# Optimization experiments

Hardware: AMD Instinct MI355X
Metric: run time of the kernel (lower is better)

The kernel has to match this reference:

```python
import jax, jax.numpy as jnp
from jax import lax
import numpy as np

B = 32768
H = 7
W = 7
EMB = 64
NUM_ACTIONS = 7
HIDDEN = 128
CNN_OUT = 64 * 3 * 3  # 576, from 7x7 input through the conv/pool stack


def setup_inputs() -> dict:
    key = jax.random.key(0)
    ks = jax.random.split(key, 20)
    frame = jax.random.randint(ks[0], (2, B, H, W, 3), 0, 11, dtype=jnp.int32)
    carried_col = jax.random.randint(ks[1], (2, B, 1), 0, 6, dtype=jnp.int32)
    carried_obj = jax.random.randint(ks[2], (2, B, 1), 0, 11, dtype=jnp.int32)

    def w(k, shape):
        return (jax.random.normal(k, shape, jnp.float32) * 0.05)

    return {
        "frame": frame,
        "carried_col": carried_col,
        "carried_obj": carried_obj,
        "conv1_w": w(ks[3], (16, 3, 2, 2)),  "conv1_b": jnp.zeros((16,), jnp.float32),
        "conv2_w": w(ks[4], (32, 16, 2, 2)), "conv2_b": jnp.zeros((32,), jnp.float32),
        "conv3_w": w(ks[5], (64, 32, 2, 2)), "conv3_b": jnp.zeros((64,), jnp.float32),
        "proj_w": w(ks[6], (EMB, CNN_OUT + 2)), "proj_b": jnp.zeros((EMB,), jnp.float32),
        "h1_w": w(ks[7], (HIDDEN, EMB * 2 + 4)), "h1_b": jnp.zeros((HIDDEN,), jnp.float32),
        "ln_g": jnp.ones((HIDDEN,), jnp.float32), "ln_b": jnp.zeros((HIDDEN,), jnp.float32),
        "h2_w": w(ks[8], (HIDDEN, HIDDEN)), "h2_b": jnp.zeros((HIDDEN,), jnp.float32),
        "h3_w": w(ks[9], (NUM_ACTIONS, HIDDEN)), "h3_b": jnp.zeros((NUM_ACTIONS,), jnp.float32),
    }


def _conv(x, wgt, b):
    # Conv2d(kernel=2, padding=1), NCHW
    y = lax.conv_general_dilated(x, wgt, (1, 1), [(1, 1), (1, 1)],
                                 dimension_numbers=("NCHW", "OIHW", "NCHW"))
    return y + b[None, :, None, None]


def _maxpool2(x):
    # MaxPool2d(2): window 2, stride 2, floor (VALID)
    return lax.reduce_window(x, -jnp.inf, lax.max, (1, 1, 2, 2), (1, 1, 2, 2), "VALID")


def _encode(fr, cc, co, p):
    x = fr.transpose(0, 3, 1, 2).astype(jnp.float32)  # [B,3,H,W]
    x = _maxpool2(jax.nn.relu(_conv(x, p["conv1_w"], p["conv1_b"])))  # [B,16,4,4]
    x = _maxpool2(jax.nn.relu(_conv(x, p["conv2_w"], p["conv2_b"])))  # [B,32,2,2]
    x = jax.nn.relu(_conv(x, p["conv3_w"], p["conv3_b"]))             # [B,64,3,3]
    feats = x.reshape(x.shape[0], -1)                                  # [B,576]
    carried = jnp.concatenate([cc, co], axis=-1).astype(jnp.float32)   # [B,2]
    comb = jnp.concatenate([feats, carried], axis=1)                   # [B,578]
    return jax.nn.relu(comb @ p["proj_w"].T + p["proj_b"])            # [B,64]


def _dir_pos(fr):
    # vectorized first-match of frame[...,0]==10 in row-major order
    b = fr.shape[0]
    mask = (fr[..., 0] == 10).reshape(b, -1)             # [B, H*W]
    has = jnp.any(mask, axis=-1)                         # [B]
    idx = jnp.argmax(mask, axis=-1)                      # first True (row-major)
    y = idx // W
    x = idx % W
    ch2 = fr[..., 2].reshape(b, -1)
    d_raw = jnp.take_along_axis(ch2, idx[:, None], axis=1)[:, 0] % 4
    d = jnp.where(has, d_raw, 0)                         # [B] int
    pos = jnp.stack([y.astype(jnp.float32) / (H - 1),
                     x.astype(jnp.float32) / (W - 1)], axis=-1)
    pos = jnp.where(has[:, None], pos, jnp.float32(0.5))  # [B,2]
    return d, pos


def _forward(frame, carried_col, carried_obj, p):
    curr_f, next_f = frame[0], frame[1]
    curr_emb = _encode(curr_f, carried_col[0], carried_obj[0], p)
    next_emb = _encode(next_f, carried_col[1], carried_obj[1], p)
    cd, cpos = _dir_pos(curr_f)
    nd, npos = _dir_pos(next_f)
    delta = ((nd - cd + 4) % 4).astype(jnp.float32)
    angle = delta * (2.0 * 3.14159 / 4.0)  # matches source constant
    dir_delta = jnp.stack([jnp.sin(angle), jnp.cos(angle)], axis=-1)  # [B,2]
    pos_delta = npos - cpos                                           # [B,2]
    comb = jnp.concatenate([curr_emb, next_emb, dir_delta, pos_delta], axis=-1)  # [B,132]
    h = comb @ p["h1_w"].T + p["h1_b"]
    mu = h.mean(-1, keepdims=True)
    var = ((h - mu) ** 2).mean(-1, keepdims=True)
    h = (h - mu) * lax.rsqrt(var + 1e-5) * p["ln_g"] + p["ln_b"]
    h = jax.nn.relu(h)  # dropout = identity in eval
    h = jax.nn.relu(h @ p["h2_w"].T + p["h2_b"])
    return h @ p["h3_w"].T + p["h3_b"]  # [B, num_actions]


def reference(frame, carried_col, carried_obj,
              conv1_w, conv1_b, conv2_w, conv2_b, conv3_w, conv3_b,
              proj_w, proj_b, h1_w, h1_b, ln_g, ln_b,
              h2_w, h2_b, h3_w, h3_b):
    p = dict(conv1_w=conv1_w, conv1_b=conv1_b, conv2_w=conv2_w, conv2_b=conv2_b,
             conv3_w=conv3_w, conv3_b=conv3_b, proj_w=proj_w, proj_b=proj_b,
             h1_w=h1_w, h1_b=h1_b, ln_g=ln_g, ln_b=ln_b,
             h2_w=h2_w, h2_b=h2_b, h3_w=h3_w, h3_b=h3_b)
    return _forward(frame, carried_col, carried_obj, p)
```

## Files before the change

### kernel.cpp

```cpp
#include <hip/hip_runtime.h>
#include <hip/hip_bf16.h>

#define BATCH 32768

typedef unsigned short u16;
typedef unsigned int u32;
typedef __attribute__((ext_vector_type(8))) short bf16x8;
typedef __attribute__((ext_vector_type(4))) float f32x4;

__device__ __forceinline__ float bf2f(u16 u) {
    union { u32 u; float f; } c; c.u = ((u32)u) << 16; return c.f;
}
__device__ __forceinline__ u16 f2bf(float f) {
    union { float f; u32 u; } c; c.f = f;
    u32 x = c.u;
    u32 r = (x + 0x7fffu + ((x >> 16) & 1u)) >> 16;
    return (u16)r;
}
__device__ __forceinline__ u16 i2bf(int v) {
    union { float f; u32 u; } c; c.f = (float)v;
    return (u16)(c.u >> 16);
}

__global__ __launch_bounds__(256) void k0_prep(const float* __restrict__ pw,
        const float* __restrict__ w2, const float* __restrict__ w3,
        const float* __restrict__ h2w, const float* __restrict__ h1w,
        const float* __restrict__ w1,
        u16* __restrict__ pwT, u16* __restrict__ w2r, u16* __restrict__ w3r,
        u16* __restrict__ h2hi, u16* __restrict__ h2lo,
        u16* __restrict__ h1hi, u16* __restrict__ h1lo,
        u16* __restrict__ w1hi, u16* __restrict__ w1lo) {
    int idx = blockIdx.x * 256 + threadIdx.x;
    if (idx < 38912) {
        int j = idx / 608, kk = idx - j * 608;
        float v = 0.f;
        if (kk < 576) {
            int p = kk >> 6, oc = kk & 63;
            v = pw[j * 578 + oc * 9 + p];
        } else if (kk < 578) {
            v = pw[j * 578 + kk];
        }
        pwT[idx] = f2bf(v);
    } else if (idx < 40960) {
        int i = idx - 38912;
        int oc = i >> 6, rem = i & 63, tap = rem >> 4, ic = rem & 15;
        w2r[i] = f2bf(w2[oc * 64 + ic * 4 + tap]);
    } else if (idx < 49152) {
        int i = idx - 40960;
        int oc = i >> 7, rem = i & 127, tap = rem >> 5, ic = rem & 31;
        w3r[i] = f2bf(w3[oc * 128 + ic * 4 + tap]);
    } else if (idx < 65536) {
        int i = idx - 49152;
        float v = h2w[i];
        u16 hi = f2bf(v);
        h2hi[i] = hi;
        h2lo[i] = f2bf(v - bf2f(hi));
    } else if (idx < 86016) {
        int i = idx - 65536;
        int j = i / 160, k = i - j * 160;
        float v = (k < 132) ? h1w[j * 132 + k] : 0.f;
        u16 hi = f2bf(v);
        h1hi[i] = hi;
        h1lo[i] = f2bf(v - bf2f(hi));
    } else if (idx < 86528) {
        int i = idx - 86016;
        int oc = i >> 5, k = i & 31;
        int ky = k >> 3, kx = (k >> 2) & 1, c = k & 3;
        float v = (ky < 2 && c < 3) ? w1[oc * 12 + c * 4 + ky * 2 + kx] : 0.f;
        u16 hi = f2bf(v);
        w1hi[i] = hi;
        w1lo[i] = f2bf(v - bf2f(hi));
    }
}

__global__ __launch_bounds__(512, 4) void kall(const int* __restrict__ frame,
        const u16* __restrict__ w1hi, const u16* __restrict__ w1lo,
        const float* __restrict__ b1,
        const u16* __restrict__ w2r, const float* __restrict__ b2,
        const u16* __restrict__ w3r, const float* __restrict__ b3,
        const int* __restrict__ ccol, const int* __restrict__ cobj,
        const u16* __restrict__ pwT, const float* __restrict__ pb,
        const u16* __restrict__ h1hi, const u16* __restrict__ h1lo,
        const float* __restrict__ h1b,
        const float* __restrict__ lng, const float* __restrict__ lnb,
        const u16* __restrict__ h2hi, const u16* __restrict__ h2lo,
        const float* __restrict__ h2b,
        const float* __restrict__ h3w, const float* __restrict__ h3b,
        float* __restrict__ out) {
    __shared__ u16 lds[22784];
    __shared__ float4 fdirL[32];
    u16* p2L    = lds;
    u16* p1L    = lds + 4096;
    u16* frL4   = lds + 12288;
    u16* featL  = lds + 4096;
    u16* combHi = lds;
    u16* combLo = lds + 2688;
    float* hL   = (float*)(lds + 5376);
    u16* hLhi   = lds + 9600;
    u16* hLlo   = lds + 12288;

    int t = threadIdx.x;
    int l = t & 63;
    int wv = t >> 6;
    int col = l & 15;
    int kg = l >> 4;
    int wq = wv & 3, wh = wv >> 2;
    int b0 = blockIdx.x * 16;

    #pragma unroll
    for (int i = 0; i < 3; ++i) {
        int o = i * 512 + t;
        if (o < 1312) *(uint4*)(frL4 + o * 8) = make_uint4(0u, 0u, 0u, 0u);
    }
    __syncthreads();

    #pragma unroll
    for (int i = 0; i < 4; ++i) {
        int c = i * 512 + t;
        if (c < 1568) {
            int le = c / 49, rem = c - le * 49;
            int y = rem / 7, x = rem - y * 7;
            const int* fp = frame
                + ((size_t)b0 + (size_t)(le & 15) + (size_t)(le >> 4) * BATCH) * 147
                + rem * 3;
            int v0 = fp[0], v1 = fp[1], v2 = fp[2];
            uint2 st;
            st.x = (u32)i2bf(v0) | ((u32)i2bf(v1) << 16);
            st.y = (u32)i2bf(v2);
            *(uint2*)(frL4 + le * 328 + (y + 1) * 36 + (x + 1) * 4) = st;
        }
    }
    __syncthreads();

    {
        bf16x8 c1hi = *(const bf16x8*)(w1hi + col * 32 + kg * 8);
        bf16x8 c1lo = *(const bf16x8*)(w1lo + col * 32 + kg * 8);
        float c1b = b1[col];
        bool wr1 = (kg < 2);
        #pragma unroll
        for (int q = 0; q < 4; ++q) {
            int le = wh * 16 + wq * 4 + q;
            const u16* eb = frL4 + le * 328;
            u16* op = p1L + le * 256;
            #pragma unroll
            for (int mt = 0; mt < 4; ++mt) {
                int posA = mt * 16 + col;
                int oy = posA >> 3, ox = posA & 7;
                bf16x8 a;
                if (kg < 2) {
                    const u16* ap = eb + (oy + kg) * 36 + ox * 4;
                    union { uint2 d[2]; bf16x8 v; } uu;
                    uu.d[0] = *(const uint2*)ap;
                    uu.d[1] = *(const uint2*)(ap + 4);
                    a = uu.v;
                } else {
                    #pragma unroll
                    for (int j = 0; j < 8; ++j) a[j] = 0;
                }
                f32x4 acc = {0.f, 0.f, 0.f, 0.f};
                acc = __builtin_amdgcn_mfma_f32_16x16x32_bf16(a, c1hi, acc, 0, 0, 0);
                acc = __builtin_amdgcn_mfma_f32_16x16x32_bf16(a, c1lo, acc, 0, 0, 0);
                float x0 = fmaxf(acc[0] + c1b, 0.f);
                float x1 = fmaxf(acc[1] + c1b, 0.f);
                float x2 = fmaxf(acc[2] + c1b, 0.f);
                float x3 = fmaxf(acc[3] + c1b, 0.f);
                float y0 = fmaxf(x0, x1);
                float y1 = fmaxf(x2, x3);
                float m0 = fmaxf(y0, __shfl_xor(y0, 32, 64));
                float m1 = fmaxf(y1, __shfl_xor(y1, 32, 64));
                if (wr1) {
                    op[(mt * 4 + kg * 2 + 0) * 16 + col] = f2bf(m0);
                    op[(mt * 4 + kg * 2 + 1) * 16 + col] = f2bf(m1);
                }
            }
        }
        {
            int e = wh * 16 + wq * 4 + kg;
            const u16* eb = frL4 + e * 328;
            int best = 49;
            #pragma unroll
            for (int q2 = 0; q2 < 4; ++q2) {
                int cell = col + q2 * 16;
                if (cell < 49) {
                    int y = cell / 7, x = cell - y * 7;
                    u16 v = eb[(y + 1) * 36 + (x + 1) * 4];
                    if (v == (u16)0x4120 && cell < best) best = cell;
                }
            }
            best = min(best, __shfl_xor(best, 1, 64));
            best = min(best, __shfl_xor(best, 2, 64));
            best = min(best, __shfl_xor(best, 4, 64));
            best = min(best, __shfl_xor(best, 8, 64));
            if (col == 0) {
                float dd = 0.f, py = 0.5f, px = 0.5f;
                if (best < 49) {
                    int y = best / 7, x = best - y * 7;
                    u16 c2 = eb[(y + 1) * 36 + (x + 1) * 4 + 2];
                    dd = (float)(((int)bf2f(c2)) & 3);
                    py = (float)y / 6.0f;
                    px = (float)x / 6.0f;
                }
                fdirL[e] = make_float4(dd, py, px, 0.f);
            }
        }
    }
    __syncthreads();

    {
        bf16x8 bfrag[2][2];
        #pragma unroll
        for (int s = 0; s < 2; ++s)
            #pragma unroll
            for (int nt = 0; nt < 2; ++nt)
                bfrag[s][nt] = *(const bf16x8*)(w2r + (nt * 16 + col) * 64 + s * 32 + kg * 8);
        float bias2[2] = { b2[col], b2[16 + col] };
        int oy = col >> 2, ox = col & 3;
        int aoff[2]; bool aok[2];
        #pragma unroll
        for (int s = 0; s < 2; ++s) {
            int tap = 2 * s + (kg >> 1);
            int ky = tap >> 1, kx = tap & 1;
            int iy = oy - 1 + ky, ix = ox - 1 + kx;
            aok[s] = (iy >= 0 && ix >= 0);
            aoff[s] = (iy * 4 + ix) * 16 + (kg & 1) * 8;
        }
        #pragma unroll
        for (int q = 0; q < 4; ++q) {
            int e = wv * 4 + q;
            const u16* pbase = p1L + e * 256;
            bf16x8 a0 = {0,0,0,0,0,0,0,0}, a1 = {0,0,0,0,0,0,0,0};
            if (aok[0]) a0 = *(const bf16x8*)(pbase + aoff[0]);
            if (aok[1]) a1 = *(const bf16x8*)(pbase + aoff[1]);
            f32x4 acc0 = {0.f,0.f,0.f,0.f}, acc1 = {0.f,0.f,0.f,0.f};
            acc0 = __builtin_amdgcn_mfma_f32_16x16x32_bf16(a0, bfrag[0][0], acc0, 0, 0, 0);
            acc1 = __builtin_amdgcn_mfma_f32_16x16x32_bf16(a0, bfrag[0][1], acc1, 0, 0, 0);
            acc0 = __builtin_amdgcn_mfma_f32_16x16x32_bf16(a1, bfrag[1][0], acc0, 0, 0, 0);
            acc1 = __builtin_amdgcn_mfma_f32_16x16x32_bf16(a1, bfrag[1][1], acc1, 0, 0, 0);
            #pragma unroll
            for (int nt = 0; nt < 2; ++nt) {
                f32x4 acc = nt ? acc1 : acc0;
                float b = bias2[nt];
                float m0 = fmaxf(fmaxf(acc[0] + b, 0.f), fmaxf(acc[1] + b, 0.f));
                float m1 = fmaxf(fmaxf(acc[2] + b, 0.f), fmaxf(acc[3] + b, 0.f));
                float p0 = fmaxf(m0, __shfl_xor(m0, 16, 64));
                float p1 = fmaxf(m1, __shfl_xor(m1, 16, 64));
                if ((kg & 1) == 0) {
                    int qq = (kg >> 1) * 2;
                    u16* op = p2L + e * 128 + nt * 16 + col;
                    op[qq * 32]       = f2bf(p0);
                    op[(qq + 1) * 32] = f2bf(p1);
                }
            }
        }
    }
    __syncthreads();

    int colhi = col >> 3, collo = col & 7;
    {
        bf16x8 bfrag[4][4];
        #pragma unroll
        for (int s = 0; s < 4; ++s)
            #pragma unroll
            for (int nt = 0; nt < 4; ++nt)
                bfrag[s][nt] = *(const bf16x8*)(w3r + (nt * 16 + col) * 128 + s * 32 + kg * 8);
        float bias[4];
        #pragma unroll
        for (int nt = 0; nt < 4; ++nt) bias[nt] = b3[nt * 16 + col];

        auto do_tile = [&](int i) {
            int m0 = i * 16;
            int m = m0 + col;
            u32 elem = (u32)(((unsigned long long)(u32)m * 954437177ull) >> 33);
            int p = m - (int)elem * 9;
            int oy = (p * 86) >> 8;
            int ox = p - 3 * oy;
            const u16* pbase = p2L + elem * 128 + kg * 8;
            f32x4 acc[4];
            #pragma unroll
            for (int nt = 0; nt < 4; ++nt) {
                acc[nt][0] = 0.f; acc[nt][1] = 0.f; acc[nt][2] = 0.f; acc[nt][3] = 0.f;
            }
            #pragma unroll
            for (int s = 0; s < 4; ++s) {
                int ky = s >> 1, kx = s & 1;
                int iy = oy - 1 + ky, ix = ox - 1 + kx;
                bf16x8 a = {0,0,0,0,0,0,0,0};
                if (iy >= 0 && iy <= 1 && ix >= 0 && ix <= 1)
                    a = *(const bf16x8*)(pbase + (iy * 2 + ix) * 32);
                #pragma unroll
                for (int nt = 0; nt < 4; ++nt)
                    acc[nt] = __builtin_amdgcn_mfma_f32_16x16x32_bf16(a, bfrag[s][nt], acc[nt], 0, 0, 0);
            }
            #pragma unroll
            for (int r = 0; r < 4; ++r) {
                int mr = m0 + kg * 4 + r;
                u32 er = (u32)(((unsigned long long)(u32)mr * 954437177ull) >> 33);
                int pr = mr - (int)er * 9;
                u16* fb = featL + er * 584 + collo;
                #pragma unroll
                for (int nt = 0; nt < 4; ++nt) {
                    int blk = pr * 8 + nt * 2 + colhi;
                    fb[blk * 8] = f2bf(fmaxf(acc[nt][r] + bias[nt], 0.f));
                }
            }
        };
        do_tile(wv);
        do_tile(8 + wv);
        if (wv < 2) do_tile(16 + wv);
    }
    if (t < 32) {
        int g = b0 + (t >> 4) * BATCH + (t & 15);
        union { u16 s[8]; uint4 q; } b;
        b.s[0] = f2bf((float)ccol[g]);
        b.s[1] = f2bf((float)cobj[g]);
        #pragma unroll
        for (int i = 2; i < 8; ++i) b.s[i] = 0;
        *(uint4*)(featL + t * 584 + 576) = b.q;
    }
    __syncthreads();

    {
        int rh = wv & 1, nf = wv >> 1;
        const u16* arowb = featL + (rh * 16 + col) * 584;
        const u16* brow  = pwT + (nf * 16 + col) * 608 + kg * 8;
        f32x4 accA = {0.f,0.f,0.f,0.f}, accB = {0.f,0.f,0.f,0.f};
        #pragma unroll
        for (int k0 = 0; k0 < 608; k0 += 32) {
            bf16x8 a;
            if (k0 + kg * 8 < 584) {
                a = *(const bf16x8*)(arowb + k0 + kg * 8);
            } else {
                #pragma unroll
                for (int j = 0; j < 8; ++j) a[j] = 0;
            }
            bf16x8 b = *(const bf16x8*)(brow + k0);
            if ((k0 >> 5) & 1)
                accB = __builtin_amdgcn_mfma_f32_16x16x32_bf16(a, b, accB, 0, 0, 0);
            else
                accA = __builtin_amdgcn_mfma_f32_16x16x32_bf16(a, b, accA, 0, 0, 0);
        }
        __syncthreads();
        if (t < 16) {
            float4 f0 = fdirL[t];
            float4 f1 = fdirL[16 + t];
            int delta = (((int)f1.x) - ((int)f0.x) + 4) & 3;
            const float ANG = (float)(2.0 * 3.14159 / 4.0);
            float ang = (float)delta * ANG;
            float xs[4] = { sinf(ang), cosf(ang), f1.y - f0.y, f1.z - f0.z };
            #pragma unroll
            for (int j = 0; j < 4; ++j) {
                u16 hi = f2bf(xs[j]);
                combHi[t * 168 + 128 + j] = hi;
                combLo[t * 168 + 128 + j] = f2bf(xs[j] - bf2f(hi));
            }
        }
        {
            int n = nf * 16 + col;
            float pbv = pb[n];
            #pragma unroll
            for (int r = 0; r < 4; ++r) {
                float v = fmaxf(accA[r] + accB[r] + pbv, 0.f);
                u16 hi = f2bf(v);
                int off = (kg * 4 + r) * 168 + rh * 64 + n;
                combHi[off] = hi;
                combLo[off] = f2bf(v - bf2f(hi));
            }
        }
    }
    __syncthreads();

    {
        const u16* ah = combHi + col * 168 + kg * 8;
        const u16* al = combLo + col * 168 + kg * 8;
        int n = wv * 16 + col;
        const u16* bh = h1hi + n * 160 + kg * 8;
        const u16* bl = h1lo + n * 160 + kg * 8;
        f32x4 accP = {0.f,0.f,0.f,0.f}, accQ = {0.f,0.f,0.f,0.f};
        #pragma unroll
        for (int s = 0; s < 5; ++s) {
            bf16x8 Ah = *(const bf16x8*)(ah + s * 32);
            bf16x8 Al = *(const bf16x8*)(al + s * 32);
            bf16x8 Bh = *(const bf16x8*)(bh + s * 32);
            bf16x8 Bl = *(const bf16x8*)(bl + s * 32);
            accP = __builtin_amdgcn_mfma_f32_16x16x32_bf16(Ah, Bh, accP, 0, 0, 0);
            accQ = __builtin_amdgcn_mfma_f32_16x16x32_bf16(Al, Bh, accQ, 0, 0, 0);
            accQ = __builtin_amdgcn_mfma_f32_16x16x32_bf16(Ah, Bl, accQ, 0, 0, 0);
        }
        float bv = h1b[n];
        #pragma unroll
        for (int r = 0; r < 4; ++r)
            hL[(kg * 4 + r) * 132 + n] = accP[r] + accQ[r] + bv;
    }
    __syncthreads();

    #pragma unroll
    for (int rr = 0; rr < 2; ++rr) {
        int row = wv * 2 + rr;
        float* rp = hL + row * 132 + l * 2;
        float2 v = *(const float2*)rp;
        float s = v.x + v.y;
        s += __shfl_xor(s, 1, 64);
        s += __shfl_xor(s, 2, 64);
        s += __shfl_xor(s, 4, 64);
        s += __shfl_xor(s, 8, 64);
        s += __shfl_xor(s, 16, 64);
        s += __shfl_xor(s, 32, 64);
        float mu = s * (1.0f / 128.0f);
        float d0 = v.x - mu, d1 = v.y - mu;
        float vs = d0 * d0 + d1 * d1;
        vs += __shfl_xor(vs, 1, 64);
        vs += __shfl_xor(vs, 2, 64);
        vs += __shfl_xor(vs, 4, 64);
        vs += __shfl_xor(vs, 8, 64);
        vs += __shfl_xor(vs, 16, 64);
        vs += __shfl_xor(vs, 32, 64);
        float rs = rsqrtf(vs * (1.0f / 128.0f) + 1e-5f);
        float o0 = fmaxf(d0 * rs * lng[l * 2]     + lnb[l * 2],     0.f);
        float o1 = fmaxf(d1 * rs * lng[l * 2 + 1] + lnb[l * 2 + 1], 0.f);
        u16 h0 = f2bf(o0), h1v = f2bf(o1);
        *(u32*)(hLhi + row * 168 + l * 2) = (u32)h0 | ((u32)h1v << 16);
        u16 l0 = f2bf(o0 - bf2f(h0)), l1v = f2bf(o1 - bf2f(h1v));
        *(u32*)(hLlo + row * 168 + l * 2) = (u32)l0 | ((u32)l1v << 16);
    }
    __syncthreads();

    {
        const u16* ah = hLhi + col * 168 + kg * 8;
        const u16* al = hLlo + col * 168 + kg * 8;
        int n = wv * 16 + col;
        const u16* bh = h2hi + n * 128 + kg * 8;
        const u16* bl = h2lo + n * 128 + kg * 8;
        f32x4 accP = {0.f,0.f,0.f,0.f}, accQ = {0.f,0.f,0.f,0.f};
        #pragma unroll
        for (int s = 0; s < 4; ++s) {
            bf16x8 Ah = *(const bf16x8*)(ah + s * 32);
            bf16x8 Al = *(const bf16x8*)(al + s * 32);
            bf16x8 Bh = *(const bf16x8*)(bh + s * 32);
            bf16x8 Bl = *(const bf16x8*)(bl + s * 32);
            accP = __builtin_amdgcn_mfma_f32_16x16x32_bf16(Ah, Bh, accP, 0, 0, 0);
            accQ = __builtin_amdgcn_mfma_f32_16x16x32_bf16(Al, Bh, accQ, 0, 0, 0);
            accQ = __builtin_amdgcn_mfma_f32_16x16x32_bf16(Ah, Bl, accQ, 0, 0, 0);
        }
        float bv = h2b[n];
        #pragma unroll
        for (int r = 0; r < 4; ++r)
            hL[(kg * 4 + r) * 132 + n] = fmaxf(accP[r] + accQ[r] + bv, 0.f);
    }
    __syncthreads();

    if (t < 112) {
        int row = t / 7, j = t - row * 7;
        const float* rp = hL + row * 132;
        const float* wr0 = h3w + j * 128;
        float a0 = h3b[j];
        #pragma unroll 4
        for (int c = 0; c < 32; ++c) {
            float4 v = *(const float4*)(rp + c * 4);
            float4 w = *(const float4*)(wr0 + c * 4);
            a0 += v.x * w.x + v.y * w.y + v.z * w.z + v.w * w.w;
        }
        out[(size_t)(b0 + row) * 7 + j] = a0;
    }
}

extern "C" void kernel_launch(void* const* d_in, const int* in_sizes, int n_in,
                              void* d_out, int out_size, void* d_ws, size_t ws_size,
                              hipStream_t stream) {
    const int*   frame = (const int*)d_in[0];
    const int*   ccol  = (const int*)d_in[1];
    const int*   cobj  = (const int*)d_in[2];
    const float* w1    = (const float*)d_in[3];
    const float* b1    = (const float*)d_in[4];
    const float* w2    = (const float*)d_in[5];
    const float* b2    = (const float*)d_in[6];
    const float* w3    = (const float*)d_in[7];
    const float* b3    = (const float*)d_in[8];
    const float* pw    = (const float*)d_in[9];
    const float* pb    = (const float*)d_in[10];
    const float* h1w   = (const float*)d_in[11];
    const float* h1b   = (const float*)d_in[12];
    const float* lng   = (const float*)d_in[13];
    const float* lnb   = (const float*)d_in[14];
    const float* h2w   = (const float*)d_in[15];
    const float* h2b   = (const float*)d_in[16];
    const float* h3w   = (const float*)d_in[17];
    const float* h3b   = (const float*)d_in[18];
    float* out = (float*)d_out;

    char* ws = (char*)d_ws;
    u16*   pwT      = (u16*)(ws + 0);
    u16*   w2r      = (u16*)(ws + 131072);
    u16*   w3r      = (u16*)(ws + 139264);
    u16*   h2hi     = (u16*)(ws + 163840);
    u16*   h2lo     = (u16*)(ws + 196608);
    u16*   h1hi     = (u16*)(ws + 229376);
    u16*   h1lo     = (u16*)(ws + 270336);
    u16*   w1hi     = (u16*)(ws + 311296);
    u16*   w1lo     = (u16*)(ws + 312320);

    k0_prep<<<340, 256, 0, stream>>>(pw, w2, w3, h2w, h1w, w1,
                                     pwT, w2r, w3r, h2hi, h2lo, h1hi, h1lo,
                                     w1hi, w1lo);
    kall<<<2048, 512, 0, stream>>>(frame, w1hi, w1lo, b1, w2r, b2,
                                   w3r, b3, ccol, cobj, pwT, pb,
                                   h1hi, h1lo, h1b, lng, lnb,
                                   h2hi, h2lo, h2b, h3w, h3b, out);
}
```

Before: 218.3 us.

## Halve block to 8 samples and 256 threads, remapping MLP MFMA tiles

```diff
diff --git a/kernel.cpp b/kernel.cpp
--- a/kernel.cpp
+++ b/kernel.cpp
@@ -73,7 +73,7 @@
     }
 }
 
-__global__ __launch_bounds__(512, 4) void kall(const int* __restrict__ frame,
+__global__ __launch_bounds__(256, 7) void kall(const int* __restrict__ frame,
         const u16* __restrict__ w1hi, const u16* __restrict__ w1lo,
         const float* __restrict__ b1,
         const u16* __restrict__ w2r, const float* __restrict__ b2,
@@ -87,41 +87,40 @@
         const float* __restrict__ h2b,
         const float* __restrict__ h3w, const float* __restrict__ h3b,
         float* __restrict__ out) {
-    __shared__ u16 lds[22784];
-    __shared__ float4 fdirL[32];
+    __shared__ u16 lds[11392];
+    __shared__ float4 fdirL[16];
     u16* p2L    = lds;
-    u16* p1L    = lds + 4096;
-    u16* frL4   = lds + 12288;
-    u16* featL  = lds + 4096;
+    u16* p1L    = lds + 2048;
+    u16* frL4   = lds + 6144;
+    u16* featL  = lds + 2048;
     u16* combHi = lds;
-    u16* combLo = lds + 2688;
-    float* hL   = (float*)(lds + 5376);
-    u16* hLhi   = lds + 9600;
-    u16* hLlo   = lds + 12288;
+    u16* combLo = lds + 1088;
+    float* hL   = (float*)(lds + 2176);
+    u16* hLhi   = lds + 4288;
+    u16* hLlo   = lds + 5376;
 
     int t = threadIdx.x;
     int l = t & 63;
     int wv = t >> 6;
     int col = l & 15;
     int kg = l >> 4;
-    int wq = wv & 3, wh = wv >> 2;
-    int b0 = blockIdx.x * 16;
+    int b0 = blockIdx.x * 8;
 
     #pragma unroll
     for (int i = 0; i < 3; ++i) {
-        int o = i * 512 + t;
-        if (o < 1312) *(uint4*)(frL4 + o * 8) = make_uint4(0u, 0u, 0u, 0u);
+        int o = i * 256 + t;
+        if (o < 656) *(uint4*)(frL4 + o * 8) = make_uint4(0u, 0u, 0u, 0u);
     }
     __syncthreads();
 
     #pragma unroll
     for (int i = 0; i < 4; ++i) {
-        int c = i * 512 + t;
-        if (c < 1568) {
+        int c = i * 256 + t;
+        if (c < 784) {
             int le = c / 49, rem = c - le * 49;
             int y = rem / 7, x = rem - y * 7;
             const int* fp = frame
-                + ((size_t)b0 + (size_t)(le & 15) + (size_t)(le >> 4) * BATCH) * 147
+                + ((size_t)b0 + (size_t)(le & 7) + (size_t)(le >> 3) * BATCH) * 147
                 + rem * 3;
             int v0 = fp[0], v1 = fp[1], v2 = fp[2];
             uint2 st;
@@ -139,7 +138,7 @@
         bool wr1 = (kg < 2);
         #pragma unroll
         for (int q = 0; q < 4; ++q) {
-            int le = wh * 16 + wq * 4 + q;
+            int le = wv * 4 + q;
             const u16* eb = frL4 + le * 328;
             u16* op = p1L + le * 256;
             #pragma unroll
@@ -175,7 +174,7 @@
             }
         }
         {
-            int e = wh * 16 + wq * 4 + kg;
+            int e = wv * 4 + kg;
             const u16* eb = frL4 + e * 328;
             int best = 49;
             #pragma unroll
@@ -305,11 +304,11 @@
             }
         };
         do_tile(wv);
-        do_tile(8 + wv);
-        if (wv < 2) do_tile(16 + wv);
-    }
-    if (t < 32) {
-        int g = b0 + (t >> 4) * BATCH + (t & 15);
+        do_tile(4 + wv);
+        if (wv == 0) do_tile(8);
+    }
+    if (t < 16) {
+        int g = b0 + (t >> 3) * BATCH + (t & 7);
         union { u16 s[8]; uint4 q; } b;
         b.s[0] = f2bf((float)ccol[g]);
         b.s[1] = f2bf((float)cobj[g]);
@@ -320,9 +319,8 @@
     __syncthreads();
 
     {
-        int rh = wv & 1, nf = wv >> 1;
-        const u16* arowb = featL + (rh * 16 + col) * 584;
-        const u16* brow  = pwT + (nf * 16 + col) * 608 + kg * 8;
+        const u16* arowb = featL + col * 584;
+        const u16* brow  = pwT + (wv * 16 + col) * 608 + kg * 8;
         f32x4 accA = {0.f,0.f,0.f,0.f}, accB = {0.f,0.f,0.f,0.f};
         #pragma unroll
         for (int k0 = 0; k0 < 608; k0 += 32) {
@@ -340,28 +338,33 @@
                 accA = __builtin_amdgcn_mfma_f32_16x16x32_bf16(a, b, accA, 0, 0, 0);
         }
         __syncthreads();
-        if (t < 16) {
+        if (t < 8) {
             float4 f0 = fdirL[t];
-            float4 f1 = fdirL[16 + t];
+            float4 f1 = fdirL[8 + t];
             int delta = (((int)f1.x) - ((int)f0.x) + 4) & 3;
             const float ANG = (float)(2.0 * 3.14159 / 4.0);
             float ang = (float)delta * ANG;
             float xs[4] = { sinf(ang), cosf(ang), f1.y - f0.y, f1.z - f0.z };
+            union { u16 s[8]; uint4 q; } bh, bl;
             #pragma unroll
             for (int j = 0; j < 4; ++j) {
                 u16 hi = f2bf(xs[j]);
-                combHi[t * 168 + 128 + j] = hi;
-                combLo[t * 168 + 128 + j] = f2bf(xs[j] - bf2f(hi));
-            }
+                bh.s[j] = hi;
+                bl.s[j] = f2bf(xs[j] - bf2f(hi));
+                bh.s[j + 4] = 0; bl.s[j + 4] = 0;
+            }
+            *(uint4*)(combHi + t * 136 + 128) = bh.q;
+            *(uint4*)(combLo + t * 136 + 128) = bl.q;
         }
         {
-            int n = nf * 16 + col;
+            int n = wv * 16 + col;
             float pbv = pb[n];
             #pragma unroll
             for (int r = 0; r < 4; ++r) {
+                int m = kg * 4 + r;
                 float v = fmaxf(accA[r] + accB[r] + pbv, 0.f);
                 u16 hi = f2bf(v);
-                int off = (kg * 4 + r) * 168 + rh * 64 + n;
+                int off = (m < 8) ? (m * 136 + n) : ((m - 8) * 136 + 64 + n);
                 combHi[off] = hi;
                 combLo[off] = f2bf(v - bf2f(hi));
             }
@@ -370,26 +373,41 @@
     __syncthreads();
 
     {
-        const u16* ah = combHi + col * 168 + kg * 8;
-        const u16* al = combLo + col * 168 + kg * 8;
-        int n = wv * 16 + col;
-        const u16* bh = h1hi + n * 160 + kg * 8;
-        const u16* bl = h1lo + n * 160 + kg * 8;
-        f32x4 accP = {0.f,0.f,0.f,0.f}, accQ = {0.f,0.f,0.f,0.f};
+        const u16* ah = combHi + col * 136 + kg * 8;
+        const u16* al = combLo + col * 136 + kg * 8;
+        f32x4 accP[2], accQ[2];
+        #pragma unroll
+        for (int nt = 0; nt < 2; ++nt) {
+            accP[nt][0]=0.f; accP[nt][1]=0.f; accP[nt][2]=0.f; accP[nt][3]=0.f;
+            accQ[nt][0]=0.f; accQ[nt][1]=0.f; accQ[nt][2]=0.f; accQ[nt][3]=0.f;
+        }
         #pragma unroll
         for (int s = 0; s < 5; ++s) {
-            bf16x8 Ah = *(const bf16x8*)(ah + s * 32);
-            bf16x8 Al = *(const bf16x8*)(al + s * 32);
-            bf16x8 Bh = *(const bf16x8*)(bh + s * 32);
-            bf16x8 Bl = *(const bf16x8*)(bl + s * 32);
-            accP = __builtin_amdgcn_mfma_f32_16x16x32_bf16(Ah, Bh, accP, 0, 0, 0);
-            accQ = __builtin_amdgcn_mfma_f32_16x16x32_bf16(Al, Bh, accQ, 0, 0, 0);
-            accQ = __builtin_amdgcn_mfma_f32_16x16x32_bf16(Ah, Bl, accQ, 0, 0, 0);
-        }
-        float bv = h1b[n];
-        #pragma unroll
-        for (int r = 0; r < 4; ++r)
-            hL[(kg * 4 + r) * 132 + n] = accP[r] + accQ[r] + bv;
+            bf16x8 Ah = {0,0,0,0,0,0,0,0}, Al = {0,0,0,0,0,0,0,0};
+            if (col < 8 && (s < 4 || kg == 0)) {
+                Ah = *(const bf16x8*)(ah + s * 32);
+                Al = *(const bf16x8*)(al + s * 32);
+            }
+            #pragma unroll
+            for (int nt = 0; nt < 2; ++nt) {
+                int n0 = (wv * 2 + nt) * 16 + col;
+                bf16x8 Bh = *(const bf16x8*)(h1hi + n0 * 160 + s * 32 + kg * 8);
+                bf16x8 Bl = *(const bf16x8*)(h1lo + n0 * 160 + s * 32 + kg * 8);
+                accP[nt] = __builtin_amdgcn_mfma_f32_16x16x32_bf16(Ah, Bh, accP[nt], 0, 0, 0);
+                accQ[nt] = __builtin_amdgcn_mfma_f32_16x16x32_bf16(Al, Bh, accQ[nt], 0, 0, 0);
+                accQ[nt] = __builtin_amdgcn_mfma_f32_16x16x32_bf16(Ah, Bl, accQ[nt], 0, 0, 0);
+            }
+        }
+        #pragma unroll
+        for (int nt = 0; nt < 2; ++nt) {
+            int n = (wv * 2 + nt) * 16 + col;
+            float bv = h1b[n];
+            if (kg < 2) {
+                #pragma unroll
+                for (int r = 0; r < 4; ++r)
+                    hL[(kg * 4 + r) * 132 + n] = accP[nt][r] + accQ[nt][r] + bv;
+            }
+        }
     }
     __syncthreads();
 
@@ -418,37 +436,52 @@
         float o0 = fmaxf(d0 * rs * lng[l * 2]     + lnb[l * 2],     0.f);
         float o1 = fmaxf(d1 * rs * lng[l * 2 + 1] + lnb[l * 2 + 1], 0.f);
         u16 h0 = f2bf(o0), h1v = f2bf(o1);
-        *(u32*)(hLhi + row * 168 + l * 2) = (u32)h0 | ((u32)h1v << 16);
+        *(u32*)(hLhi + row * 136 + l * 2) = (u32)h0 | ((u32)h1v << 16);
         u16 l0 = f2bf(o0 - bf2f(h0)), l1v = f2bf(o1 - bf2f(h1v));
-        *(u32*)(hLlo + row * 168 + l * 2) = (u32)l0 | ((u32)l1v << 16);
+        *(u32*)(hLlo + row * 136 + l * 2) = (u32)l0 | ((u32)l1v << 16);
     }
     __syncthreads();
 
     {
-        const u16* ah = hLhi + col * 168 + kg * 8;
-        const u16* al = hLlo + col * 168 + kg * 8;
-        int n = wv * 16 + col;
-        const u16* bh = h2hi + n * 128 + kg * 8;
-        const u16* bl = h2lo + n * 128 + kg * 8;
-        f32x4 accP = {0.f,0.f,0.f,0.f}, accQ = {0.f,0.f,0.f,0.f};
+        const u16* ah = hLhi + col * 136 + kg * 8;
+        const u16* al = hLlo + col * 136 + kg * 8;
+        f32x4 accP[2], accQ[2];
+        #pragma unroll
+        for (int nt = 0; nt < 2; ++nt) {
+            accP[nt][0]=0.f; accP[nt][1]=0.f; accP[nt][2]=0.f; accP[nt][3]=0.f;
+            accQ[nt][0]=0.f; accQ[nt][1]=0.f; accQ[nt][2]=0.f; accQ[nt][3]=0.f;
+        }
         #pragma unroll
         for (int s = 0; s < 4; ++s) {
-            bf16x8 Ah = *(const bf16x8*)(ah + s * 32);
-            bf16x8 Al = *(const bf16x8*)(al + s * 32);
-            bf16x8 Bh = *(const bf16x8*)(bh + s * 32);
-            bf16x8 Bl = *(const bf16x8*)(bl + s * 32);
-            accP = __builtin_amdgcn_mfma_f32_16x16x32_bf16(Ah, Bh, accP, 0, 0, 0);
-            accQ = __builtin_amdgcn_mfma_f32_16x16x32_bf16(Al, Bh, accQ, 0, 0, 0);
-            accQ = __builtin_amdgcn_mfma_f32_16x16x32_bf16(Ah, Bl, accQ, 0, 0, 0);
-        }
-        float bv = h2b[n];
-        #pragma unroll
-        for (int r = 0; r < 4; ++r)
-            hL[(kg * 4 + r) * 132 + n] = fmaxf(accP[r] + accQ[r] + bv, 0.f);
-    }
-    __syncthreads();
-
-    if (t < 112) {
+            bf16x8 Ah = {0,0,0,0,0,0,0,0}, Al = {0,0,0,0,0,0,0,0};
+            if (col < 8) {
+                Ah = *(const bf16x8*)(ah + s * 32);
+                Al = *(const bf16x8*)(al + s * 32);
+            }
+            #pragma unroll
+            for (int nt = 0; nt < 2; ++nt) {
+                int n0 = (wv * 2 + nt) * 16 + col;
+                bf16x8 Bh = *(const bf16x8*)(h2hi + n0 * 128 + s * 32 + kg * 8);
+                bf16x8 Bl = *(const bf16x8*)(h2lo + n0 * 128 + s * 32 + kg * 8);
+                accP[nt] = __builtin_amdgcn_mfma_f32_16x16x32_bf16(Ah, Bh, accP[nt], 0, 0, 0);
+                accQ[nt] = __builtin_amdgcn_mfma_f32_16x16x32_bf16(Al, Bh, accQ[nt], 0, 0, 0);
+                accQ[nt] = __builtin_amdgcn_mfma_f32_16x16x32_bf16(Ah, Bl, accQ[nt], 0, 0, 0);
+            }
+        }
+        #pragma unroll
+        for (int nt = 0; nt < 2; ++nt) {
+            int n = (wv * 2 + nt) * 16 + col;
+            float bv = h2b[n];
+            if (kg < 2) {
+                #pragma unroll
+                for (int r = 0; r < 4; ++r)
+                    hL[(kg * 4 + r) * 132 + n] = fmaxf(accP[nt][r] + accQ[nt][r] + bv, 0.f);
+            }
+        }
+    }
+    __syncthreads();
+
+    if (t < 56) {
         int row = t / 7, j = t - row * 7;
         const float* rp = hL + row * 132;
         const float* wr0 = h3w + j * 128;
@@ -501,7 +534,7 @@
     k0_prep<<<340, 256, 0, stream>>>(pw, w2, w3, h2w, h1w, w1,
                                      pwT, w2r, w3r, h2hi, h2lo, h1hi, h1lo,
                                      w1hi, w1lo);
-    kall<<<2048, 512, 0, stream>>>(frame, w1hi, w1lo, b1, w2r, b2,
+    kall<<<4096, 256, 0, stream>>>(frame, w1hi, w1lo, b1, w2r, b2,
                                    w3r, b3, ccol, cobj, pwT, pb,
                                    h1hi, h1lo, h1b, lng, lnb,
                                    h2hi, h2lo, h2b, h3w, h3b, out);
```

Measured after the change: 303.8 us. 39.2% more time.
